# Kernel tuning notes

Measured on AMD Instinct MI355X. Metric: run time of the kernel, lower is better.

The kernel has to match this reference:

```python
import jax, jax.numpy as jnp
import numpy as np

B, S, N, U, E, L = 32, 32, 128, 64, 2, 2
N_STEPS = 3
NUM_CLASSES = 5


def setup_inputs() -> dict:
    key = jax.random.key(0)
    ks = jax.random.split(key, 10)
    input_seq = jax.random.normal(ks[0], (B, S, N * U), dtype=jnp.float32)
    seq_lengths = jax.random.randint(ks[1], (B,), 0, S)
    # per-edge-type adjacency, scaled ~row-stochastic for numerical sanity
    adjacency_matrix = jax.random.uniform(ks[2], (B, E, N, N), dtype=jnp.float32) / N
    sc = 1.0 / np.sqrt(U)
    W_msg = jax.random.normal(ks[3], (L, E, U, U), dtype=jnp.float32) * sc
    b_msg = jnp.zeros((L, U), dtype=jnp.float32)
    Wg = jax.random.normal(ks[4], (L, 3, U, U), dtype=jnp.float32) * sc  # gates from aggregated messages
    Ug = jax.random.normal(ks[5], (L, 3, U, U), dtype=jnp.float32) * sc  # gates from hidden state
    bg = jnp.zeros((L, 3, U), dtype=jnp.float32)
    fc_w = jax.random.normal(ks[6], (U, NUM_CLASSES), dtype=jnp.float32) * sc
    fc_b = jnp.zeros((NUM_CLASSES,), dtype=jnp.float32)
    return {
        "input_seq": input_seq, "seq_lengths": seq_lengths,
        "adjacency_matrix": adjacency_matrix,
        "W_msg": W_msg, "b_msg": b_msg, "Wg": Wg, "Ug": Ug, "bg": bg,
        "fc_w": fc_w, "fc_b": fc_b,
    }


def _ggnn_layer(h, A, W_msg_l, b_msg_l, Wg_l, Ug_l, bg_l):
    # h: [S,B,N,U], A: [B,E,N,N] (shared across timesteps)
    for _ in range(N_STEPS):
        # typed message passing: sum_e A_e @ h @ W_e
        a = jnp.einsum('benm,sbmu,euv->sbnv', A, h, W_msg_l) + b_msg_l
        g_a = jnp.einsum('sbnu,guv->gsbnv', a, Wg_l)  # [3,S,B,N,U]
        z = jax.nn.sigmoid(g_a[0] + h @ Ug_l[0] + bg_l[0])
        r = jax.nn.sigmoid(g_a[1] + h @ Ug_l[1] + bg_l[1])
        c = jnp.tanh(g_a[2] + (r * h) @ Ug_l[2] + bg_l[2])
        h = (1.0 - z) * h + z * c
    return h


def reference(input_seq, seq_lengths, adjacency_matrix, W_msg, b_msg, Wg, Ug, bg, fc_w, fc_b):
    # encoder: hidden state is NOT carried across timesteps in the original
    # (cell is called with current input only), so timesteps are vectorized.
    cur = input_seq.reshape(B, S, N, U).transpose(1, 0, 2, 3)  # [S,B,N,U]
    for l in range(L):
        cur = _ggnn_layer(cur, adjacency_matrix, W_msg[l], b_msg[l], Wg[l], Ug[l], bg[l])
    out = cur.transpose(1, 0, 2, 3)  # [B,S,N,U]
    idx = jnp.clip(seq_lengths - 1, 0, S - 1)
    last = out[jnp.arange(B), idx]  # [B,N,U] (last relevant timestep)
    # dropout is identity in eval mode
    logits = jax.nn.relu(last) @ fc_w + fc_b  # [B,N,C]
    return jnp.max(logits, axis=1)  # [B,C]
```

## Files before the change

### kernel.cpp

```cpp
#include <hip/hip_runtime.h>

#define B 32
#define S 32
#define N 128
#define U 64
#define E 2
#define NCLS 5


__device__ __forceinline__ float sigmoid_f(float x) {
    return __fdividef(1.f, 1.f + __expf(-x));
}
__device__ __forceinline__ float tanh_f(float x) {
    float t = __expf(-2.f * fabsf(x));
    float y = __fdividef(1.f - t, 1.f + t);
    return copysignf(y, x);
}
__device__ __forceinline__ float bcast(float v, int u) {
    return __uint_as_float(__builtin_amdgcn_readlane(__float_as_uint(v), u));
}

template <int FIRST, int LAST>
__global__ __launch_bounds__(256) void k_step(
    const float* __restrict__ x, const int* __restrict__ lens,
    const float* __restrict__ hin, float* __restrict__ hout,
    const float* __restrict__ A, const float* __restrict__ Wmsg,
    const float* __restrict__ bmsg, const float* __restrict__ Wg,
    const float* __restrict__ Ug, const float* __restrict__ bg,
    const float* __restrict__ fcw, float* __restrict__ partial, int l) {
    __shared__ float red[4 * NCLS];
    int tid = threadIdx.x;
    int wave = tid >> 6, lane = tid & 63;
    int b = blockIdx.x >> 4;
    int j = blockIdx.x & 15;
    int n0 = __builtin_amdgcn_readfirstlane(j * 8 + wave * 2);

    const float* __restrict__ hsrc;
    if (FIRST) {
        int idx = lens[b] - 1;
        idx = idx < 0 ? 0 : (idx > S - 1 ? S - 1 : idx);
        hsrc = x + (size_t)(b * S + idx) * N * U;
    } else {
        hsrc = hin + (size_t)b * N * U;
    }

    float hv0 = hsrc[(n0 + 0) * U + lane];
    float hv1 = hsrc[(n0 + 1) * U + lane];

    float s00 = 0.f, s01 = 0.f, s10 = 0.f, s11 = 0.f;
    {
        const float4* A00 = (const float4*)(A + (((size_t)b * E + 0) * N + n0 + 0) * N);
        const float4* A10 = (const float4*)(A + (((size_t)b * E + 0) * N + n0 + 1) * N);
        const float4* A01 = (const float4*)(A + (((size_t)b * E + 1) * N + n0 + 0) * N);
        const float4* A11 = (const float4*)(A + (((size_t)b * E + 1) * N + n0 + 1) * N);
#pragma unroll 8
        for (int m4 = 0; m4 < N / 4; ++m4) {
            float4 a00 = A00[m4], a10 = A10[m4], a01 = A01[m4], a11 = A11[m4];
            float q0 = hsrc[(m4 * 4 + 0) * U + lane];
            float q1 = hsrc[(m4 * 4 + 1) * U + lane];
            float q2 = hsrc[(m4 * 4 + 2) * U + lane];
            float q3 = hsrc[(m4 * 4 + 3) * U + lane];
            s00 = fmaf(a00.x, q0, s00); s00 = fmaf(a00.y, q1, s00);
            s00 = fmaf(a00.z, q2, s00); s00 = fmaf(a00.w, q3, s00);
            s10 = fmaf(a10.x, q0, s10); s10 = fmaf(a10.y, q1, s10);
            s10 = fmaf(a10.z, q2, s10); s10 = fmaf(a10.w, q3, s10);
            s01 = fmaf(a01.x, q0, s01); s01 = fmaf(a01.y, q1, s01);
            s01 = fmaf(a01.z, q2, s01); s01 = fmaf(a01.w, q3, s01);
            s11 = fmaf(a11.x, q0, s11); s11 = fmaf(a11.y, q1, s11);
            s11 = fmaf(a11.z, q2, s11); s11 = fmaf(a11.w, q3, s11);
        }
    }

    float bm = bmsg[l * U + lane];
    float av0 = bm, av1 = bm;
    {
        const float* W0 = Wmsg + (size_t)(l * E + 0) * U * U + lane;
        const float* W1 = W0 + U * U;
#pragma unroll 16
        for (int u = 0; u < U; ++u) {
            float w = W0[u * U];
            av0 = fmaf(bcast(s00, u), w, av0);
            av1 = fmaf(bcast(s10, u), w, av1);
        }
#pragma unroll 16
        for (int u = 0; u < U; ++u) {
            float w = W1[u * U];
            av0 = fmaf(bcast(s01, u), w, av0);
            av1 = fmaf(bcast(s11, u), w, av1);
        }
    }

    const float* Wg0 = Wg + (size_t)l * 3 * U * U + lane;
    const float* Wg1 = Wg0 + U * U;
    const float* Wg2 = Wg1 + U * U;
    const float* Ug0 = Ug + (size_t)l * 3 * U * U + lane;
    const float* Ug1 = Ug0 + U * U;
    const float* Ug2 = Ug1 + U * U;
    float accz0 = bg[(l * 3 + 0) * U + lane], accz1 = accz0;
    float accr0 = bg[(l * 3 + 1) * U + lane], accr1 = accr0;
    float accc0 = bg[(l * 3 + 2) * U + lane], accc1 = accc0;
#pragma unroll 16
    for (int u = 0; u < U; ++u) {
        float w0 = Wg0[u * U], w1 = Wg1[u * U], w2 = Wg2[u * U];
        float g0 = Ug0[u * U], g1 = Ug1[u * U];
        float a0 = bcast(av0, u), a1 = bcast(av1, u);
        float h0 = bcast(hv0, u), h1 = bcast(hv1, u);
        accz0 = fmaf(a0, w0, accz0); accz0 = fmaf(h0, g0, accz0);
        accz1 = fmaf(a1, w0, accz1); accz1 = fmaf(h1, g0, accz1);
        accr0 = fmaf(a0, w1, accr0); accr0 = fmaf(h0, g1, accr0);
        accr1 = fmaf(a1, w1, accr1); accr1 = fmaf(h1, g1, accr1);
        accc0 = fmaf(a0, w2, accc0);
        accc1 = fmaf(a1, w2, accc1);
    }
    float rg0 = sigmoid_f(accr0), rg1 = sigmoid_f(accr1);
    float rh0 = rg0 * hv0, rh1 = rg1 * hv1;
#pragma unroll 16
    for (int u = 0; u < U; ++u) {
        float g2 = Ug2[u * U];
        accc0 = fmaf(bcast(rh0, u), g2, accc0);
        accc1 = fmaf(bcast(rh1, u), g2, accc1);
    }
    float zg0 = sigmoid_f(accz0), zg1 = sigmoid_f(accz1);
    float hn0 = (1.f - zg0) * hv0 + zg0 * tanh_f(accc0);
    float hn1 = (1.f - zg1) * hv1 + zg1 * tanh_f(accc1);

    if (!LAST) {
        hout[((size_t)b * N + n0 + 0) * U + lane] = hn0;
        hout[((size_t)b * N + n0 + 1) * U + lane] = hn1;
    } else {
        float lg0[NCLS], lg1[NCLS];
        float rv0 = hn0 > 0.f ? hn0 : 0.f;
        float rv1 = hn1 > 0.f ? hn1 : 0.f;
#pragma unroll
        for (int c = 0; c < NCLS; c++) {
            float w = fcw[lane * NCLS + c];
            lg0[c] = rv0 * w;
            lg1[c] = rv1 * w;
        }
#pragma unroll
        for (int off = 32; off; off >>= 1) {
#pragma unroll
            for (int c = 0; c < NCLS; c++) {
                lg0[c] += __shfl_xor(lg0[c], off, 64);
                lg1[c] += __shfl_xor(lg1[c], off, 64);
            }
        }
        if (lane == 0) {
#pragma unroll
            for (int c = 0; c < NCLS; c++) red[wave * NCLS + c] = fmaxf(lg0[c], lg1[c]);
        }
        __syncthreads();
        if (tid < NCLS) {
            float m = red[tid];
            for (int w = 1; w < 4; ++w) m = fmaxf(m, red[w * NCLS + tid]);
            partial[(size_t)(b * 16 + j) * NCLS + tid] = m;
        }
    }
}

__global__ void k_final(const float* __restrict__ partial, const float* __restrict__ fcb,
                        float* __restrict__ out) {
    int b = blockIdx.x, c = threadIdx.x;
    if (c < NCLS) {
        float m = -3.4e38f;
        for (int jj = 0; jj < 16; ++jj)
            m = fmaxf(m, partial[(size_t)(b * 16 + jj) * NCLS + c]);
        out[b * NCLS + c] = m + fcb[c];
    }
}

extern "C" void kernel_launch(void* const* d_in, const int* in_sizes, int n_in,
                              void* d_out, int out_size, void* d_ws, size_t ws_size,
                              hipStream_t stream) {
    const float* x    = (const float*)d_in[0];
    const int*   lens = (const int*)d_in[1];
    const float* A    = (const float*)d_in[2];
    const float* Wmsg = (const float*)d_in[3];
    const float* bmsg = (const float*)d_in[4];
    const float* Wg   = (const float*)d_in[5];
    const float* Ug   = (const float*)d_in[6];
    const float* bg   = (const float*)d_in[7];
    const float* fcw  = (const float*)d_in[8];
    const float* fcb  = (const float*)d_in[9];
    float* out = (float*)d_out;

    float* hA      = (float*)d_ws;
    float* hB      = hA + (size_t)B * N * U;
    float* partial = hB + (size_t)B * N * U;

    k_step<1, 0><<<B * 16, 256, 0, stream>>>(x, lens, nullptr, hA, A, Wmsg, bmsg, Wg, Ug, bg, fcw, partial, 0);
    k_step<0, 0><<<B * 16, 256, 0, stream>>>(x, lens, hA, hB, A, Wmsg, bmsg, Wg, Ug, bg, fcw, partial, 0);
    k_step<0, 0><<<B * 16, 256, 0, stream>>>(x, lens, hB, hA, A, Wmsg, bmsg, Wg, Ug, bg, fcw, partial, 0);
    k_step<0, 0><<<B * 16, 256, 0, stream>>>(x, lens, hA, hB, A, Wmsg, bmsg, Wg, Ug, bg, fcw, partial, 1);
    k_step<0, 0><<<B * 16, 256, 0, stream>>>(x, lens, hB, hA, A, Wmsg, bmsg, Wg, Ug, bg, fcw, partial, 1);
    k_step<0, 1><<<B * 16, 256, 0, stream>>>(x, lens, hA, hB, A, Wmsg, bmsg, Wg, Ug, bg, fcw, partial, 1);
    k_final<<<B, 64, 0, stream>>>(partial, fcb, out);
}
```

Measured before the change: 209.2 us.

## Fuse all GGNN steps and final reduction into one cooperative kernel with grid sync

Replaces the seven separate kernel launches (six step kernels plus the final max) with a single cooperative kernel. The kernel loops over the six propagation steps, ping-ponging hidden states between two buffers, and uses grid-wide synchronization between steps. The final class max is done at the end by the first B blocks. This is meant to remove per-launch overhead and gaps between launches. In exchange it adds grid-sync cost, requires all 512 blocks to be co-resident, and the launch_bounds hint may constrain register allocation.

```diff
diff --git a/kernel.cpp b/kernel.cpp
--- a/kernel.cpp
+++ b/kernel.cpp
@@ -1,4 +1,7 @@
 #include <hip/hip_runtime.h>
+#include <hip/hip_cooperative_groups.h>
+
+namespace cg = cooperative_groups;
 
 #define B 32
 #define S 32
@@ -20,14 +23,15 @@
     return __uint_as_float(__builtin_amdgcn_readlane(__float_as_uint(v), u));
 }
 
-template <int FIRST, int LAST>
-__global__ __launch_bounds__(256) void k_step(
+__global__ __launch_bounds__(256, 2) void k_fused(
     const float* __restrict__ x, const int* __restrict__ lens,
-    const float* __restrict__ hin, float* __restrict__ hout,
+    float* __restrict__ hA, float* __restrict__ hB,
     const float* __restrict__ A, const float* __restrict__ Wmsg,
     const float* __restrict__ bmsg, const float* __restrict__ Wg,
     const float* __restrict__ Ug, const float* __restrict__ bg,
-    const float* __restrict__ fcw, float* __restrict__ partial, int l) {
+    const float* __restrict__ fcw, const float* __restrict__ fcb,
+    float* __restrict__ partial, float* __restrict__ out) {
+    cg::grid_group grid = cg::this_grid();
     __shared__ float red[4 * NCLS];
     int tid = threadIdx.x;
     int wave = tid >> 6, lane = tid & 63;
@@ -35,24 +39,26 @@
     int j = blockIdx.x & 15;
     int n0 = __builtin_amdgcn_readfirstlane(j * 8 + wave * 2);
 
-    const float* __restrict__ hsrc;
-    if (FIRST) {
-        int idx = lens[b] - 1;
-        idx = idx < 0 ? 0 : (idx > S - 1 ? S - 1 : idx);
-        hsrc = x + (size_t)(b * S + idx) * N * U;
-    } else {
-        hsrc = hin + (size_t)b * N * U;
-    }
-
-    float hv0 = hsrc[(n0 + 0) * U + lane];
-    float hv1 = hsrc[(n0 + 1) * U + lane];
-
-    float s00 = 0.f, s01 = 0.f, s10 = 0.f, s11 = 0.f;
-    {
-        const float4* A00 = (const float4*)(A + (((size_t)b * E + 0) * N + n0 + 0) * N);
-        const float4* A10 = (const float4*)(A + (((size_t)b * E + 0) * N + n0 + 1) * N);
-        const float4* A01 = (const float4*)(A + (((size_t)b * E + 1) * N + n0 + 0) * N);
-        const float4* A11 = (const float4*)(A + (((size_t)b * E + 1) * N + n0 + 1) * N);
+    int idx = lens[b] - 1;
+    idx = idx < 0 ? 0 : (idx > S - 1 ? S - 1 : idx);
+    const float* xsrc = x + (size_t)(b * S + idx) * N * U;
+
+    const float4* A00 = (const float4*)(A + (((size_t)b * E + 0) * N + n0 + 0) * N);
+    const float4* A10 = (const float4*)(A + (((size_t)b * E + 0) * N + n0 + 1) * N);
+    const float4* A01 = (const float4*)(A + (((size_t)b * E + 1) * N + n0 + 0) * N);
+    const float4* A11 = (const float4*)(A + (((size_t)b * E + 1) * N + n0 + 1) * N);
+
+#pragma unroll 1
+    for (int step = 0; step < 6; ++step) {
+        int l = step >= 3 ? 1 : 0;
+        const float* hsrc = (step == 0) ? xsrc
+                                        : ((step & 1) ? hA : hB) + (size_t)b * N * U;
+        float* hdst = ((step & 1) ? hB : hA) + ((size_t)b * N + n0) * U;
+
+        float hv0 = hsrc[(n0 + 0) * U + lane];
+        float hv1 = hsrc[(n0 + 1) * U + lane];
+
+        float s00 = 0.f, s01 = 0.f, s10 = 0.f, s11 = 0.f;
 #pragma unroll 8
         for (int m4 = 0; m4 < N / 4; ++m4) {
             float4 a00 = A00[m4], a10 = A10[m4], a01 = A01[m4], a11 = A11[m4];
@@ -69,103 +75,101 @@
             s11 = fmaf(a11.x, q0, s11); s11 = fmaf(a11.y, q1, s11);
             s11 = fmaf(a11.z, q2, s11); s11 = fmaf(a11.w, q3, s11);
         }
+
+        float bm = bmsg[l * U + lane];
+        float av0 = bm, av1 = bm;
+        {
+            const float* W0 = Wmsg + (size_t)(l * E + 0) * U * U + lane;
+            const float* W1 = W0 + U * U;
+#pragma unroll 16
+            for (int u = 0; u < U; ++u) {
+                float w = W0[u * U];
+                av0 = fmaf(bcast(s00, u), w, av0);
+                av1 = fmaf(bcast(s10, u), w, av1);
+            }
+#pragma unroll 16
+            for (int u = 0; u < U; ++u) {
+                float w = W1[u * U];
+                av0 = fmaf(bcast(s01, u), w, av0);
+                av1 = fmaf(bcast(s11, u), w, av1);
+            }
+        }
+
+        const float* Wg0 = Wg + (size_t)l * 3 * U * U + lane;
+        const float* Wg1 = Wg0 + U * U;
+        const float* Wg2 = Wg1 + U * U;
+        const float* Ug0 = Ug + (size_t)l * 3 * U * U + lane;
+        const float* Ug1 = Ug0 + U * U;
+        const float* Ug2 = Ug1 + U * U;
+        float accz0 = bg[(l * 3 + 0) * U + lane], accz1 = accz0;
+        float accr0 = bg[(l * 3 + 1) * U + lane], accr1 = accr0;
+        float accc0 = bg[(l * 3 + 2) * U + lane], accc1 = accc0;
+#pragma unroll 16
+        for (int u = 0; u < U; ++u) {
+            float w0 = Wg0[u * U], w1 = Wg1[u * U], w2 = Wg2[u * U];
+            float g0 = Ug0[u * U], g1 = Ug1[u * U];
+            float a0 = bcast(av0, u), a1 = bcast(av1, u);
+            float h0 = bcast(hv0, u), h1 = bcast(hv1, u);
+            accz0 = fmaf(a0, w0, accz0); accz0 = fmaf(h0, g0, accz0);
+            accz1 = fmaf(a1, w0, accz1); accz1 = fmaf(h1, g0, accz1);
+            accr0 = fmaf(a0, w1, accr0); accr0 = fmaf(h0, g1, accr0);
+            accr1 = fmaf(a1, w1, accr1); accr1 = fmaf(h1, g1, accr1);
+            accc0 = fmaf(a0, w2, accc0);
+            accc1 = fmaf(a1, w2, accc1);
+        }
+        float rg0 = sigmoid_f(accr0), rg1 = sigmoid_f(accr1);
+        float rh0 = rg0 * hv0, rh1 = rg1 * hv1;
+#pragma unroll 16
+        for (int u = 0; u < U; ++u) {
+            float g2 = Ug2[u * U];
+            accc0 = fmaf(bcast(rh0, u), g2, accc0);
+            accc1 = fmaf(bcast(rh1, u), g2, accc1);
+        }
+        float zg0 = sigmoid_f(accz0), zg1 = sigmoid_f(accz1);
+        float hn0 = (1.f - zg0) * hv0 + zg0 * tanh_f(accc0);
+        float hn1 = (1.f - zg1) * hv1 + zg1 * tanh_f(accc1);
+
+        if (step < 5) {
+            hdst[lane] = hn0;
+            hdst[U + lane] = hn1;
+        } else {
+            float lg0[NCLS], lg1[NCLS];
+            float rv0 = hn0 > 0.f ? hn0 : 0.f;
+            float rv1 = hn1 > 0.f ? hn1 : 0.f;
+#pragma unroll
+            for (int c = 0; c < NCLS; c++) {
+                float w = fcw[lane * NCLS + c];
+                lg0[c] = rv0 * w;
+                lg1[c] = rv1 * w;
+            }
+#pragma unroll
+            for (int off = 32; off; off >>= 1) {
+#pragma unroll
+                for (int c = 0; c < NCLS; c++) {
+                    lg0[c] += __shfl_xor(lg0[c], off, 64);
+                    lg1[c] += __shfl_xor(lg1[c], off, 64);
+                }
+            }
+            if (lane == 0) {
+#pragma unroll
+                for (int c = 0; c < NCLS; c++) red[wave * NCLS + c] = fmaxf(lg0[c], lg1[c]);
+            }
+            __syncthreads();
+            if (tid < NCLS) {
+                float m = red[tid];
+                for (int w = 1; w < 4; ++w) m = fmaxf(m, red[w * NCLS + tid]);
+                partial[(size_t)(b * 16 + j) * NCLS + tid] = m;
+            }
+        }
+        grid.sync();
     }
 
-    float bm = bmsg[l * U + lane];
-    float av0 = bm, av1 = bm;
-    {
-        const float* W0 = Wmsg + (size_t)(l * E + 0) * U * U + lane;
-        const float* W1 = W0 + U * U;
-#pragma unroll 16
-        for (int u = 0; u < U; ++u) {
-            float w = W0[u * U];
-            av0 = fmaf(bcast(s00, u), w, av0);
-            av1 = fmaf(bcast(s10, u), w, av1);
-        }
-#pragma unroll 16
-        for (int u = 0; u < U; ++u) {
-            float w = W1[u * U];
-            av0 = fmaf(bcast(s01, u), w, av0);
-            av1 = fmaf(bcast(s11, u), w, av1);
-        }
-    }
-
-    const float* Wg0 = Wg + (size_t)l * 3 * U * U + lane;
-    const float* Wg1 = Wg0 + U * U;
-    const float* Wg2 = Wg1 + U * U;
-    const float* Ug0 = Ug + (size_t)l * 3 * U * U + lane;
-    const float* Ug1 = Ug0 + U * U;
-    const float* Ug2 = Ug1 + U * U;
-    float accz0 = bg[(l * 3 + 0) * U + lane], accz1 = accz0;
-    float accr0 = bg[(l * 3 + 1) * U + lane], accr1 = accr0;
-    float accc0 = bg[(l * 3 + 2) * U + lane], accc1 = accc0;
-#pragma unroll 16
-    for (int u = 0; u < U; ++u) {
-        float w0 = Wg0[u * U], w1 = Wg1[u * U], w2 = Wg2[u * U];
-        float g0 = Ug0[u * U], g1 = Ug1[u * U];
-        float a0 = bcast(av0, u), a1 = bcast(av1, u);
-        float h0 = bcast(hv0, u), h1 = bcast(hv1, u);
-        accz0 = fmaf(a0, w0, accz0); accz0 = fmaf(h0, g0, accz0);
-        accz1 = fmaf(a1, w0, accz1); accz1 = fmaf(h1, g0, accz1);
-        accr0 = fmaf(a0, w1, accr0); accr0 = fmaf(h0, g1, accr0);
-        accr1 = fmaf(a1, w1, accr1); accr1 = fmaf(h1, g1, accr1);
-        accc0 = fmaf(a0, w2, accc0);
-        accc1 = fmaf(a1, w2, accc1);
-    }
-    float rg0 = sigmoid_f(accr0), rg1 = sigmoid_f(accr1);
-    float rh0 = rg0 * hv0, rh1 = rg1 * hv1;
-#pragma unroll 16
-    for (int u = 0; u < U; ++u) {
-        float g2 = Ug2[u * U];
-        accc0 = fmaf(bcast(rh0, u), g2, accc0);
-        accc1 = fmaf(bcast(rh1, u), g2, accc1);
-    }
-    float zg0 = sigmoid_f(accz0), zg1 = sigmoid_f(accz1);
-    float hn0 = (1.f - zg0) * hv0 + zg0 * tanh_f(accc0);
-    float hn1 = (1.f - zg1) * hv1 + zg1 * tanh_f(accc1);
-
-    if (!LAST) {
-        hout[((size_t)b * N + n0 + 0) * U + lane] = hn0;
-        hout[((size_t)b * N + n0 + 1) * U + lane] = hn1;
-    } else {
-        float lg0[NCLS], lg1[NCLS];
-        float rv0 = hn0 > 0.f ? hn0 : 0.f;
-        float rv1 = hn1 > 0.f ? hn1 : 0.f;
-#pragma unroll
-        for (int c = 0; c < NCLS; c++) {
-            float w = fcw[lane * NCLS + c];
-            lg0[c] = rv0 * w;
-            lg1[c] = rv1 * w;
-        }
-#pragma unroll
-        for (int off = 32; off; off >>= 1) {
-#pragma unroll
-            for (int c = 0; c < NCLS; c++) {
-                lg0[c] += __shfl_xor(lg0[c], off, 64);
-                lg1[c] += __shfl_xor(lg1[c], off, 64);
-            }
-        }
-        if (lane == 0) {
-#pragma unroll
-            for (int c = 0; c < NCLS; c++) red[wave * NCLS + c] = fmaxf(lg0[c], lg1[c]);
-        }
-        __syncthreads();
-        if (tid < NCLS) {
-            float m = red[tid];
-            for (int w = 1; w < 4; ++w) m = fmaxf(m, red[w * NCLS + tid]);
-            partial[(size_t)(b * 16 + j) * NCLS + tid] = m;
-        }
-    }
-}
-
-__global__ void k_final(const float* __restrict__ partial, const float* __restrict__ fcb,
-                        float* __restrict__ out) {
-    int b = blockIdx.x, c = threadIdx.x;
-    if (c < NCLS) {
+    if (blockIdx.x < B && tid < NCLS) {
+        int bb = blockIdx.x, c = tid;
         float m = -3.4e38f;
         for (int jj = 0; jj < 16; ++jj)
-            m = fmaxf(m, partial[(size_t)(b * 16 + jj) * NCLS + c]);
-        out[b * NCLS + c] = m + fcb[c];
+            m = fmaxf(m, partial[(size_t)(bb * 16 + jj) * NCLS + c]);
+        out[bb * NCLS + c] = m + fcb[c];
     }
 }
 
@@ -188,11 +192,10 @@
     float* hB      = hA + (size_t)B * N * U;
     float* partial = hB + (size_t)B * N * U;
 
-    k_step<1, 0><<<B * 16, 256, 0, stream>>>(x, lens, nullptr, hA, A, Wmsg, bmsg, Wg, Ug, bg, fcw, partial, 0);
-    k_step<0, 0><<<B * 16, 256, 0, stream>>>(x, lens, hA, hB, A, Wmsg, bmsg, Wg, Ug, bg, fcw, partial, 0);
-    k_step<0, 0><<<B * 16, 256, 0, stream>>>(x, lens, hB, hA, A, Wmsg, bmsg, Wg, Ug, bg, fcw, partial, 0);
-    k_step<0, 0><<<B * 16, 256, 0, stream>>>(x, lens, hA, hB, A, Wmsg, bmsg, Wg, Ug, bg, fcw, partial, 1);
-    k_step<0, 0><<<B * 16, 256, 0, stream>>>(x, lens, hB, hA, A, Wmsg, bmsg, Wg, Ug, bg, fcw, partial, 1);
-    k_step<0, 1><<<B * 16, 256, 0, stream>>>(x, lens, hA, hB, A, Wmsg, bmsg, Wg, Ug, bg, fcw, partial, 1);
-    k_final<<<B, 64, 0, stream>>>(partial, fcb, out);
-}
+    void* args[] = {(void*)&x, (void*)&lens, (void*)&hA, (void*)&hB,
+                    (void*)&A, (void*)&Wmsg, (void*)&bmsg, (void*)&Wg,
+                    (void*)&Ug, (void*)&bg, (void*)&fcw, (void*)&fcb,
+                    (void*)&partial, (void*)&out};
+    hipLaunchCooperativeKernel((const void*)k_fused, dim3(B * 16), dim3(256),
+                               args, 0, stream);
+}
```

Result: slower. 501.2 us (+139.5%).

## Split each GGNN step's reductions across two waves per node pair

Applied to the files above, without the earlier changes.

Doubles the block size to 512 threads so that each node pair is handled by two waves. Each wave covers half of the adjacency reduction range and half of the U dimension in the weight matmuls, and partial sums are combined through shared memory with block barriers. The aim is to shorten the serial per-wave dependency chains and raise the number of resident waves on this latency-bound kernel. The cost is four extra __syncthreads, extra LDS traffic, and duplicated gate and elementwise work in both waves.

```diff
diff --git a/kernel.cpp b/kernel.cpp
--- a/kernel.cpp
+++ b/kernel.cpp
@@ -21,19 +21,27 @@
 }
 
 template <int FIRST, int LAST>
-__global__ __launch_bounds__(256) void k_step(
+__global__ __launch_bounds__(512, 2) void k_step(
     const float* __restrict__ x, const int* __restrict__ lens,
     const float* __restrict__ hin, float* __restrict__ hout,
     const float* __restrict__ A, const float* __restrict__ Wmsg,
     const float* __restrict__ bmsg, const float* __restrict__ Wg,
     const float* __restrict__ Ug, const float* __restrict__ bg,
     const float* __restrict__ fcw, float* __restrict__ partial, int l) {
+    __shared__ float sred[4][2][2][2][64];
+    __shared__ float avred[4][2][2][64];
+    __shared__ float gred[4][2][3][2][64];
+    __shared__ float c2red[4][2][2][64];
     __shared__ float red[4 * NCLS];
     int tid = threadIdx.x;
     int wave = tid >> 6, lane = tid & 63;
+    int g = wave & 3;
+    int k = wave >> 2;
     int b = blockIdx.x >> 4;
     int j = blockIdx.x & 15;
-    int n0 = __builtin_amdgcn_readfirstlane(j * 8 + wave * 2);
+    int n0 = __builtin_amdgcn_readfirstlane(j * 8 + g * 2);
+    int u0 = __builtin_amdgcn_readfirstlane(k * 32);
+    int m0 = __builtin_amdgcn_readfirstlane(k * 64);
 
     const float* __restrict__ hsrc;
     if (FIRST) {
@@ -49,17 +57,17 @@
 
     float s00 = 0.f, s01 = 0.f, s10 = 0.f, s11 = 0.f;
     {
-        const float4* A00 = (const float4*)(A + (((size_t)b * E + 0) * N + n0 + 0) * N);
-        const float4* A10 = (const float4*)(A + (((size_t)b * E + 0) * N + n0 + 1) * N);
-        const float4* A01 = (const float4*)(A + (((size_t)b * E + 1) * N + n0 + 0) * N);
-        const float4* A11 = (const float4*)(A + (((size_t)b * E + 1) * N + n0 + 1) * N);
+        const float4* A00 = (const float4*)(A + (((size_t)b * E + 0) * N + n0 + 0) * N + m0);
+        const float4* A10 = (const float4*)(A + (((size_t)b * E + 0) * N + n0 + 1) * N + m0);
+        const float4* A01 = (const float4*)(A + (((size_t)b * E + 1) * N + n0 + 0) * N + m0);
+        const float4* A11 = (const float4*)(A + (((size_t)b * E + 1) * N + n0 + 1) * N + m0);
 #pragma unroll 8
-        for (int m4 = 0; m4 < N / 4; ++m4) {
+        for (int m4 = 0; m4 < 16; ++m4) {
             float4 a00 = A00[m4], a10 = A10[m4], a01 = A01[m4], a11 = A11[m4];
-            float q0 = hsrc[(m4 * 4 + 0) * U + lane];
-            float q1 = hsrc[(m4 * 4 + 1) * U + lane];
-            float q2 = hsrc[(m4 * 4 + 2) * U + lane];
-            float q3 = hsrc[(m4 * 4 + 3) * U + lane];
+            float q0 = hsrc[(m0 + m4 * 4 + 0) * U + lane];
+            float q1 = hsrc[(m0 + m4 * 4 + 1) * U + lane];
+            float q2 = hsrc[(m0 + m4 * 4 + 2) * U + lane];
+            float q3 = hsrc[(m0 + m4 * 4 + 3) * U + lane];
             s00 = fmaf(a00.x, q0, s00); s00 = fmaf(a00.y, q1, s00);
             s00 = fmaf(a00.z, q2, s00); s00 = fmaf(a00.w, q3, s00);
             s10 = fmaf(a10.x, q0, s10); s10 = fmaf(a10.y, q1, s10);
@@ -70,25 +78,42 @@
             s11 = fmaf(a11.z, q2, s11); s11 = fmaf(a11.w, q3, s11);
         }
     }
-
-    float bm = bmsg[l * U + lane];
-    float av0 = bm, av1 = bm;
+    sred[g][k][0][0][lane] = s00;
+    sred[g][k][0][1][lane] = s01;
+    sred[g][k][1][0][lane] = s10;
+    sred[g][k][1][1][lane] = s11;
+    __syncthreads();
+    s00 = sred[g][0][0][0][lane] + sred[g][1][0][0][lane];
+    s01 = sred[g][0][0][1][lane] + sred[g][1][0][1][lane];
+    s10 = sred[g][0][1][0][lane] + sred[g][1][1][0][lane];
+    s11 = sred[g][0][1][1][lane] + sred[g][1][1][1][lane];
+
+    float av0, av1;
     {
+        float bm = (k == 0) ? bmsg[l * U + lane] : 0.f;
+        av0 = bm; av1 = bm;
         const float* W0 = Wmsg + (size_t)(l * E + 0) * U * U + lane;
         const float* W1 = W0 + U * U;
 #pragma unroll 16
-        for (int u = 0; u < U; ++u) {
+        for (int uu = 0; uu < 32; ++uu) {
+            int u = u0 + uu;
             float w = W0[u * U];
             av0 = fmaf(bcast(s00, u), w, av0);
             av1 = fmaf(bcast(s10, u), w, av1);
         }
 #pragma unroll 16
-        for (int u = 0; u < U; ++u) {
+        for (int uu = 0; uu < 32; ++uu) {
+            int u = u0 + uu;
             float w = W1[u * U];
             av0 = fmaf(bcast(s01, u), w, av0);
             av1 = fmaf(bcast(s11, u), w, av1);
         }
     }
+    avred[g][k][0][lane] = av0;
+    avred[g][k][1][lane] = av1;
+    __syncthreads();
+    av0 = avred[g][0][0][lane] + avred[g][1][0][lane];
+    av1 = avred[g][0][1][lane] + avred[g][1][1][lane];
 
     const float* Wg0 = Wg + (size_t)l * 3 * U * U + lane;
     const float* Wg1 = Wg0 + U * U;
@@ -96,37 +121,65 @@
     const float* Ug0 = Ug + (size_t)l * 3 * U * U + lane;
     const float* Ug1 = Ug0 + U * U;
     const float* Ug2 = Ug1 + U * U;
-    float accz0 = bg[(l * 3 + 0) * U + lane], accz1 = accz0;
-    float accr0 = bg[(l * 3 + 1) * U + lane], accr1 = accr0;
-    float accc0 = bg[(l * 3 + 2) * U + lane], accc1 = accc0;
+    float accz0, accz1, accr0, accr1, accc0, accc1;
+    {
+        float bz = (k == 0) ? bg[(l * 3 + 0) * U + lane] : 0.f;
+        float br = (k == 0) ? bg[(l * 3 + 1) * U + lane] : 0.f;
+        float bcc = (k == 0) ? bg[(l * 3 + 2) * U + lane] : 0.f;
+        accz0 = bz; accz1 = bz;
+        accr0 = br; accr1 = br;
+        accc0 = bcc; accc1 = bcc;
+#pragma unroll 8
+        for (int uu = 0; uu < 32; ++uu) {
+            int u = u0 + uu;
+            float w0 = Wg0[u * U], w1 = Wg1[u * U], w2 = Wg2[u * U];
+            float g0 = Ug0[u * U], g1 = Ug1[u * U];
+            float a0 = bcast(av0, u), a1 = bcast(av1, u);
+            float h0 = bcast(hv0, u), h1 = bcast(hv1, u);
+            accz0 = fmaf(a0, w0, accz0); accz0 = fmaf(h0, g0, accz0);
+            accz1 = fmaf(a1, w0, accz1); accz1 = fmaf(h1, g0, accz1);
+            accr0 = fmaf(a0, w1, accr0); accr0 = fmaf(h0, g1, accr0);
+            accr1 = fmaf(a1, w1, accr1); accr1 = fmaf(h1, g1, accr1);
+            accc0 = fmaf(a0, w2, accc0);
+            accc1 = fmaf(a1, w2, accc1);
+        }
+    }
+    gred[g][k][0][0][lane] = accz0; gred[g][k][0][1][lane] = accz1;
+    gred[g][k][1][0][lane] = accr0; gred[g][k][1][1][lane] = accr1;
+    gred[g][k][2][0][lane] = accc0; gred[g][k][2][1][lane] = accc1;
+    __syncthreads();
+    accz0 = gred[g][0][0][0][lane] + gred[g][1][0][0][lane];
+    accz1 = gred[g][0][0][1][lane] + gred[g][1][0][1][lane];
+    accr0 = gred[g][0][1][0][lane] + gred[g][1][1][0][lane];
+    accr1 = gred[g][0][1][1][lane] + gred[g][1][1][1][lane];
+    accc0 = gred[g][0][2][0][lane] + gred[g][1][2][0][lane];
+    accc1 = gred[g][0][2][1][lane] + gred[g][1][2][1][lane];
+
+    float rh0 = sigmoid_f(accr0) * hv0;
+    float rh1 = sigmoid_f(accr1) * hv1;
+    float c20 = 0.f, c21 = 0.f;
 #pragma unroll 16
-    for (int u = 0; u < U; ++u) {
-        float w0 = Wg0[u * U], w1 = Wg1[u * U], w2 = Wg2[u * U];
-        float g0 = Ug0[u * U], g1 = Ug1[u * U];
-        float a0 = bcast(av0, u), a1 = bcast(av1, u);
-        float h0 = bcast(hv0, u), h1 = bcast(hv1, u);
-        accz0 = fmaf(a0, w0, accz0); accz0 = fmaf(h0, g0, accz0);
-        accz1 = fmaf(a1, w0, accz1); accz1 = fmaf(h1, g0, accz1);
-        accr0 = fmaf(a0, w1, accr0); accr0 = fmaf(h0, g1, accr0);
-        accr1 = fmaf(a1, w1, accr1); accr1 = fmaf(h1, g1, accr1);
-        accc0 = fmaf(a0, w2, accc0);
-        accc1 = fmaf(a1, w2, accc1);
-    }
-    float rg0 = sigmoid_f(accr0), rg1 = sigmoid_f(accr1);
-    float rh0 = rg0 * hv0, rh1 = rg1 * hv1;
-#pragma unroll 16
-    for (int u = 0; u < U; ++u) {
+    for (int uu = 0; uu < 32; ++uu) {
+        int u = u0 + uu;
         float g2 = Ug2[u * U];
-        accc0 = fmaf(bcast(rh0, u), g2, accc0);
-        accc1 = fmaf(bcast(rh1, u), g2, accc1);
-    }
+        c20 = fmaf(bcast(rh0, u), g2, c20);
+        c21 = fmaf(bcast(rh1, u), g2, c21);
+    }
+    c2red[g][k][0][lane] = c20;
+    c2red[g][k][1][lane] = c21;
+    __syncthreads();
+    accc0 += c2red[g][0][0][lane] + c2red[g][1][0][lane];
+    accc1 += c2red[g][0][1][lane] + c2red[g][1][1][lane];
+
     float zg0 = sigmoid_f(accz0), zg1 = sigmoid_f(accz1);
     float hn0 = (1.f - zg0) * hv0 + zg0 * tanh_f(accc0);
     float hn1 = (1.f - zg1) * hv1 + zg1 * tanh_f(accc1);
 
     if (!LAST) {
-        hout[((size_t)b * N + n0 + 0) * U + lane] = hn0;
-        hout[((size_t)b * N + n0 + 1) * U + lane] = hn1;
+        if (k == 0) {
+            hout[((size_t)b * N + n0 + 0) * U + lane] = hn0;
+            hout[((size_t)b * N + n0 + 1) * U + lane] = hn1;
+        }
     } else {
         float lg0[NCLS], lg1[NCLS];
         float rv0 = hn0 > 0.f ? hn0 : 0.f;
@@ -145,9 +198,9 @@
                 lg1[c] += __shfl_xor(lg1[c], off, 64);
             }
         }
-        if (lane == 0) {
-#pragma unroll
-            for (int c = 0; c < NCLS; c++) red[wave * NCLS + c] = fmaxf(lg0[c], lg1[c]);
+        if (k == 0 && lane == 0) {
+#pragma unroll
+            for (int c = 0; c < NCLS; c++) red[g * NCLS + c] = fmaxf(lg0[c], lg1[c]);
         }
         __syncthreads();
         if (tid < NCLS) {
@@ -188,11 +241,11 @@
     float* hB      = hA + (size_t)B * N * U;
     float* partial = hB + (size_t)B * N * U;
 
-    k_step<1, 0><<<B * 16, 256, 0, stream>>>(x, lens, nullptr, hA, A, Wmsg, bmsg, Wg, Ug, bg, fcw, partial, 0);
-    k_step<0, 0><<<B * 16, 256, 0, stream>>>(x, lens, hA, hB, A, Wmsg, bmsg, Wg, Ug, bg, fcw, partial, 0);
-    k_step<0, 0><<<B * 16, 256, 0, stream>>>(x, lens, hB, hA, A, Wmsg, bmsg, Wg, Ug, bg, fcw, partial, 0);
-    k_step<0, 0><<<B * 16, 256, 0, stream>>>(x, lens, hA, hB, A, Wmsg, bmsg, Wg, Ug, bg, fcw, partial, 1);
-    k_step<0, 0><<<B * 16, 256, 0, stream>>>(x, lens, hB, hA, A, Wmsg, bmsg, Wg, Ug, bg, fcw, partial, 1);
-    k_step<0, 1><<<B * 16, 256, 0, stream>>>(x, lens, hA, hB, A, Wmsg, bmsg, Wg, Ug, bg, fcw, partial, 1);
+    k_step<1, 0><<<B * 16, 512, 0, stream>>>(x, lens, nullptr, hA, A, Wmsg, bmsg, Wg, Ug, bg, fcw, partial, 0);
+    k_step<0, 0><<<B * 16, 512, 0, stream>>>(x, lens, hA, hB, A, Wmsg, bmsg, Wg, Ug, bg, fcw, partial, 0);
+    k_step<0, 0><<<B * 16, 512, 0, stream>>>(x, lens, hB, hA, A, Wmsg, bmsg, Wg, Ug, bg, fcw, partial, 0);
+    k_step<0, 0><<<B * 16, 512, 0, stream>>>(x, lens, hA, hB, A, Wmsg, bmsg, Wg, Ug, bg, fcw, partial, 1);
+    k_step<0, 0><<<B * 16, 512, 0, stream>>>(x, lens, hB, hA, A, Wmsg, bmsg, Wg, Ug, bg, fcw, partial, 1);
+    k_step<0, 1><<<B * 16, 512, 0, stream>>>(x, lens, hA, hB, A, Wmsg, bmsg, Wg, Ug, bg, fcw, partial, 1);
     k_final<<<B, 64, 0, stream>>>(partial, fcb, out);
 }
```

Measured after the change: 195.4 us (median of 2 runs). 6.6% less time.
